# Optimization experiments

Measured on AMD Instinct MI355X. Metric: run time of the kernel, lower is better.

## Reference

```python
import jax, jax.numpy as jnp
import numpy as np

INF = 8192   # infeatures
OUTF = 8192  # outfeatures
NOUT = 64    # outlierfeatures


def setup_inputs() -> dict:
    key = jax.random.key(0)
    ks = jax.random.split(key, 7)
    x = jax.random.normal(ks[0], (1, 1, INF), dtype=jnp.float32)
    qweight = jax.random.randint(ks[1], (INF // 32 * 3, OUTF), 0, 2147483647, dtype=jnp.int32)
    scales = jax.random.uniform(ks[2], (OUTF, 1), dtype=jnp.float32) + 0.01
    zeros = jax.random.normal(ks[3], (OUTF, 1), dtype=jnp.float32)
    bias = jax.random.normal(ks[4], (OUTF,), dtype=jnp.float32)
    oweight = jax.random.normal(ks[5], (OUTF, NOUT), dtype=jnp.float32)
    outlieridx = jnp.sort(jax.random.randint(ks[6], (NOUT,), 0, INF, dtype=jnp.int32))
    return {"x": x, "qweight": qweight, "scales": scales, "zeros": zeros,
            "bias": bias, "oweight": oweight, "outlieridx": outlieridx}


def _unpack3(qweight):
    """Unpack GPTQ 3-bit layout: 3 packed int32 rows -> 32 weights. Returns [in, out] uint32 in [0,8)."""
    out = qweight.shape[1]
    q = qweight.astype(jnp.uint32).reshape(-1, 3, out)  # [nblocks, 3, out]
    r0, r1, r2 = q[:, 0], q[:, 1], q[:, 2]
    j = jnp.arange(10, dtype=jnp.uint32)
    seven = jnp.uint32(7)
    a = (r0[:, None, :] >> (3 * j)[None, :, None]) & seven            # weights 0..9
    v10 = ((r0 >> 30) & jnp.uint32(3)) | ((r1 & jnp.uint32(1)) << 2)  # weight 10 (split r0/r1)
    b = (r1[:, None, :] >> (3 * j + 1)[None, :, None]) & seven        # weights 11..20
    v21 = ((r1 >> 31) & jnp.uint32(1)) | ((r2 & jnp.uint32(3)) << 1)  # weight 21 (split r1/r2)
    c = (r2[:, None, :] >> (3 * j + 2)[None, :, None]) & seven        # weights 22..31
    vals = jnp.concatenate([a, v10[:, None, :], b, v21[:, None, :], c], axis=1)  # [nb, 32, out]
    return vals.reshape(-1, out)  # [in, out]


def reference(x, qweight, scales, zeros, bias, oweight, outlieridx):
    outshape = list(x.shape)
    outshape[-1] = scales.shape[0]
    xf = x.reshape(-1).astype(jnp.float32)  # single token [in]
    q = _unpack3(qweight).astype(jnp.float32)            # [in, out]
    W = q * scales[:, 0][None, :] - zeros[:, 0][None, :]  # dequant: scale*q - (zero*scale)
    y = xf @ W                                            # main int3 matvec -> [out]
    x_out = xf[outlieridx]                                # [noutlier]
    y = y + oweight @ x_out                               # outlier correction
    y = y + bias
    return y.astype(x.dtype).reshape(outshape)
```

## Files before the change

### kernel.cpp

```cpp
#include <hip/hip_runtime.h>
#include <stdint.h>

#define INF    8192
#define OUTF   8192
#define NOUT   64
#define NG     256
#define BLK    512
#define COLS   32
#define KC     16
#define GPT    (NG / KC)

__global__ __launch_bounds__(BLK) void q3gemv(
    const float* __restrict__ x,
    const int*   __restrict__ qw,
    const float* __restrict__ scales,
    const float* __restrict__ zeros,
    const float* __restrict__ bias,
    const float* __restrict__ ow,
    const int*   __restrict__ oidx,
    float*       __restrict__ out)
{
    __shared__ __align__(16) float xs[INF];
    __shared__ float psum[KC][COLS];
    __shared__ float xo[NOUT];
    __shared__ float wsum[BLK / 64];

    const int t     = threadIdx.x;
    const int col   = t & (COLS - 1);
    const int kc    = t >> 5;
    const int obase = blockIdx.x * COLS;

    float lsum = 0.f;
    const float4* xv = (const float4*)x;
    #pragma unroll
    for (int k = 0; k < INF / (BLK * 4); ++k) {
        float4 v = xv[t + k * BLK];
        ((float4*)xs)[t + k * BLK] = v;
        lsum += (v.x + v.y) + (v.z + v.w);
    }
    #pragma unroll
    for (int off = 32; off > 0; off >>= 1)
        lsum += __shfl_down(lsum, off, 64);
    if ((t & 63) == 0) wsum[t >> 6] = lsum;
    __syncthreads();

    if (t < NOUT) xo[t] = xs[oidx[t]];

    const unsigned* qp = (const unsigned*)qw + (size_t)(kc * GPT * 3) * OUTF + (obase + col);
    const float*    xg = xs + kc * GPT * 32;

    unsigned r0 = qp[0], r1 = qp[OUTF], r2 = qp[2 * OUTF];
    float acc[4] = {0.f, 0.f, 0.f, 0.f};

    #pragma unroll 4
    for (int gg = 0; gg < GPT; ++gg) {
        const unsigned* qn = qp + ((gg + 1 < GPT) ? (size_t)3 * OUTF : 0);
        unsigned n0 = qn[0], n1 = qn[OUTF], n2 = qn[2 * OUTF];

        float xr[32];
        #pragma unroll
        for (int j = 0; j < 8; ++j) {
            float4 tv = ((const float4*)xg)[j];
            xr[4 * j + 0] = tv.x; xr[4 * j + 1] = tv.y;
            xr[4 * j + 2] = tv.z; xr[4 * j + 3] = tv.w;
        }

        #pragma unroll
        for (int i = 0; i < 32; ++i) {
            unsigned qv;
            if (i < 10)       qv = (r0 >> (3 * i)) & 7u;
            else if (i == 10) qv = ((r0 >> 30) & 3u) | ((r1 & 1u) << 2);
            else if (i < 21)  qv = (r1 >> (3 * (i - 11) + 1)) & 7u;
            else if (i == 21) qv = ((r1 >> 31) & 1u) | ((r2 & 3u) << 1);
            else              qv = (r2 >> (3 * (i - 22) + 2)) & 7u;
            acc[i & 3] += xr[i] * (float)qv;
        }

        r0 = n0; r1 = n1; r2 = n2;
        qp += (size_t)3 * OUTF;
        xg += 32;
    }
    psum[kc][col] = (acc[0] + acc[1]) + (acc[2] + acc[3]);
    __syncthreads();

    if (t < COLS) {
        const int oo = obase + t;
        float a = 0.f;
        #pragma unroll
        for (int k = 0; k < KC; ++k) a += psum[k][t];

        float sx = 0.f;
        #pragma unroll
        for (int w = 0; w < BLK / 64; ++w) sx += wsum[w];

        float od = 0.f;
        const float4* wv = (const float4*)(ow + (size_t)oo * NOUT);
        #pragma unroll
        for (int b = 0; b < 16; ++b) {
            float4 u = wv[b];
            od += u.x * xo[4 * b + 0] + u.y * xo[4 * b + 1]
                + u.z * xo[4 * b + 2] + u.w * xo[4 * b + 3];
        }

        out[oo] = scales[oo] * a - zeros[oo] * sx + bias[oo] + od;
    }
}

extern "C" void kernel_launch(void* const* d_in, const int* in_sizes, int n_in,
                              void* d_out, int out_size, void* d_ws, size_t ws_size,
                              hipStream_t stream) {
    const float* x  = (const float*)d_in[0];
    const int*   qw = (const int*)d_in[1];
    const float* sc = (const float*)d_in[2];
    const float* zr = (const float*)d_in[3];
    const float* bs = (const float*)d_in[4];
    const float* ow = (const float*)d_in[5];
    const int*   oi = (const int*)d_in[6];
    float*       y  = (float*)d_out;

    q3gemv<<<OUTF / COLS, BLK, 0, stream>>>(x, qw, sc, zr, bs, ow, oi, y);
}
```

Baseline: 88.50 us.

## Process two output columns per thread with uint2 loads and padded shared x

Each thread now handles two adjacent output columns, loading packed weights as uint2, so each x vector read from shared memory is reused across two columns. The K dimension is split into 32 chunks instead of 16 so the block still has 512 threads. The shared x buffer is padded every 64 float4 to avoid bank conflicts between the k-chunks read by different thread groups, and psum gets one column of padding. This cuts shared-memory traffic per multiply-add and widens global loads, at the cost of more registers per thread and a larger final reduction.

```diff
diff --git a/kernel.cpp b/kernel.cpp
--- a/kernel.cpp
+++ b/kernel.cpp
@@ -7,8 +7,26 @@
 #define NG     256
 #define BLK    512
 #define COLS   32
-#define KC     16
+#define CP     16
+#define KC     32
 #define GPT    (NG / KC)
+
+#define XS4N   (INF / 4 + INF / 256)
+
+__device__ __forceinline__ void unpack_mac(unsigned r0, unsigned r1, unsigned r2,
+                                           const float* xr, float& a0, float& a1) {
+    #pragma unroll
+    for (int i = 0; i < 32; ++i) {
+        unsigned qv;
+        if (i < 10)       qv = (r0 >> (3 * i)) & 7u;
+        else if (i == 10) qv = ((r0 >> 30) & 3u) | ((r1 & 1u) << 2);
+        else if (i < 21)  qv = (r1 >> (3 * (i - 11) + 1)) & 7u;
+        else if (i == 21) qv = ((r1 >> 31) & 1u) | ((r2 & 3u) << 1);
+        else              qv = (r2 >> (3 * (i - 22) + 2)) & 7u;
+        if (i & 1) a1 += xr[i] * (float)qv;
+        else       a0 += xr[i] * (float)qv;
+    }
+}
 
 __global__ __launch_bounds__(BLK) void q3gemv(
     const float* __restrict__ x,
@@ -20,23 +38,24 @@
     const int*   __restrict__ oidx,
     float*       __restrict__ out)
 {
-    __shared__ __align__(16) float xs[INF];
-    __shared__ float psum[KC][COLS];
+    __shared__ __align__(16) float4 xs4[XS4N];
+    __shared__ float psum[KC][COLS + 1];
     __shared__ float xo[NOUT];
     __shared__ float wsum[BLK / 64];
 
     const int t     = threadIdx.x;
-    const int col   = t & (COLS - 1);
-    const int kc    = t >> 5;
+    const int cp    = t & (CP - 1);
+    const int kc    = t >> 4;
     const int obase = blockIdx.x * COLS;
 
     float lsum = 0.f;
     const float4* xv = (const float4*)x;
     #pragma unroll
     for (int k = 0; k < INF / (BLK * 4); ++k) {
-        float4 v = xv[t + k * BLK];
-        ((float4*)xs)[t + k * BLK] = v;
-        lsum += (v.x + v.y) + (v.z + v.w);
+        int v = t + k * BLK;
+        float4 d = xv[v];
+        xs4[v + (v >> 6)] = d;
+        lsum += (d.x + d.y) + (d.z + d.w);
     }
     #pragma unroll
     for (int off = 32; off > 0; off >>= 1)
@@ -44,43 +63,42 @@
     if ((t & 63) == 0) wsum[t >> 6] = lsum;
     __syncthreads();
 
-    if (t < NOUT) xo[t] = xs[oidx[t]];
+    if (t < NOUT) {
+        int i = oidx[t];
+        xo[t] = ((const float*)xs4)[i + ((i >> 8) << 2)];
+    }
 
-    const unsigned* qp = (const unsigned*)qw + (size_t)(kc * GPT * 3) * OUTF + (obase + col);
-    const float*    xg = xs + kc * GPT * 32;
+    const unsigned* qp = (const unsigned*)qw + (size_t)(kc * GPT * 3) * OUTF + (obase + 2 * cp);
+    uint2 c0 = *(const uint2*)qp;
+    uint2 c1 = *(const uint2*)(qp + OUTF);
+    uint2 c2 = *(const uint2*)(qp + 2 * OUTF);
 
-    unsigned r0 = qp[0], r1 = qp[OUTF], r2 = qp[2 * OUTF];
-    float acc[4] = {0.f, 0.f, 0.f, 0.f};
+    float aA0 = 0.f, aA1 = 0.f, aB0 = 0.f, aB1 = 0.f;
+    const int xbase = kc * 65;
 
-    #pragma unroll 4
+    #pragma unroll 2
     for (int gg = 0; gg < GPT; ++gg) {
         const unsigned* qn = qp + ((gg + 1 < GPT) ? (size_t)3 * OUTF : 0);
-        unsigned n0 = qn[0], n1 = qn[OUTF], n2 = qn[2 * OUTF];
+        uint2 n0 = *(const uint2*)qn;
+        uint2 n1 = *(const uint2*)(qn + OUTF);
+        uint2 n2 = *(const uint2*)(qn + 2 * OUTF);
 
         float xr[32];
         #pragma unroll
         for (int j = 0; j < 8; ++j) {
-            float4 tv = ((const float4*)xg)[j];
-            xr[4 * j + 0] = tv.x; xr[4 * j + 1] = tv.y;
-            xr[4 * j + 2] = tv.z; xr[4 * j + 3] = tv.w;
+            float4 d = xs4[xbase + gg * 8 + j];
+            xr[4 * j + 0] = d.x; xr[4 * j + 1] = d.y;
+            xr[4 * j + 2] = d.z; xr[4 * j + 3] = d.w;
         }
 
-        #pragma unroll
-        for (int i = 0; i < 32; ++i) {
-            unsigned qv;
-            if (i < 10)       qv = (r0 >> (3 * i)) & 7u;
-            else if (i == 10) qv = ((r0 >> 30) & 3u) | ((r1 & 1u) << 2);
-            else if (i < 21)  qv = (r1 >> (3 * (i - 11) + 1)) & 7u;
-            else if (i == 21) qv = ((r1 >> 31) & 1u) | ((r2 & 3u) << 1);
-            else              qv = (r2 >> (3 * (i - 22) + 2)) & 7u;
-            acc[i & 3] += xr[i] * (float)qv;
-        }
+        unpack_mac(c0.x, c1.x, c2.x, xr, aA0, aA1);
+        unpack_mac(c0.y, c1.y, c2.y, xr, aB0, aB1);
 
-        r0 = n0; r1 = n1; r2 = n2;
+        c0 = n0; c1 = n1; c2 = n2;
         qp += (size_t)3 * OUTF;
-        xg += 32;
     }
-    psum[kc][col] = (acc[0] + acc[1]) + (acc[2] + acc[3]);
+    psum[kc][2 * cp + 0] = aA0 + aA1;
+    psum[kc][2 * cp + 1] = aB0 + aB1;
     __syncthreads();
 
     if (t < COLS) {
```

New measurement: 91.23 us. +3.1%, slower.
